# Performance work log

Measured on AMD Instinct MI355X. Metric: run time of the kernel, lower is better.

Reference implementation:

```python
import jax, jax.numpy as jnp
import numpy as np

EPS = 1e-6  # torch.nn.PairwiseDistance default eps, added to the difference vector


def setup_inputs() -> dict:
    key = jax.random.key(0)
    k1, k2, k3 = jax.random.split(key, 3)
    B, L1, L2, D = 4, 4096, 4096, 3
    contour1 = jax.random.normal(k1, (B, L1, D), dtype=jnp.float32)
    contour2 = jax.random.normal(k2, (B, L2, D), dtype=jnp.float32)
    resolution = jax.random.uniform(k3, (1,), dtype=jnp.float32)
    return {"contour1": contour1, "contour2": contour2, "resolution": resolution}


def reference(contour1, contour2, resolution):
    # torch PairwiseDistance(2): dist = ||x1 - x2 + eps||_2 with x1 from contour1,
    # x2 from contour2. Expand ||c1 - c2 + eps||^2 =
    #   ||c1||^2 + ||c2||^2 - 2 c1.c2 + 2*eps*(sum(c1) - sum(c2)) + D*eps^2
    # to avoid materializing the [B, L2, L1, D] repeated tensors.
    D = contour1.shape[-1]
    s1 = jnp.sum(contour1 * contour1, axis=-1)          # [B, L1]
    s2 = jnp.sum(contour2 * contour2, axis=-1)          # [B, L2]
    sum1 = jnp.sum(contour1, axis=-1)                   # [B, L1]
    sum2 = jnp.sum(contour2, axis=-1)                   # [B, L2]
    cross = jnp.einsum('bmd,bld->bml', contour2, contour1)  # [B, L2, L1]
    dist2 = (s2[:, :, None] + s1[:, None, :] - 2.0 * cross
             + 2.0 * EPS * (sum1[:, None, :] - sum2[:, :, None])
             + D * EPS * EPS)
    dist = jnp.sqrt(jnp.maximum(dist2, 0.0))            # [B, L2, L1]
    min_dist = jnp.min(dist, axis=2)                    # [B, L2]
    return jnp.mean(min_dist * resolution, axis=1)      # [B]
```

## Files before the change

kernel.cpp:

```cpp
#include <hip/hip_runtime.h>
#include <math.h>

#define EPS 1e-6f
#define FLT_BIG 3.402823466e+38f

constexpr int BLK = 256;
constexpr int MPT = 8;
constexpr int NCHUNK = 64;
constexpr int NMB = 2;
constexpr int CLK = 64;

__global__ void __launch_bounds__(BLK)
k_min(const float* __restrict__ c1, const float* __restrict__ c2,
      float* __restrict__ part, float* __restrict__ out, int L1, int L2) {
    __shared__ float4 tile[CLK];

    const int mb = blockIdx.x, chunk = blockIdx.y, b = blockIdx.z;
    const int tid = threadIdx.x;

    if (mb == 0 && chunk == 0 && tid == 0) out[b] = 0.0f;

    const int l0 = chunk * CLK;
    const float* src = c1 + ((size_t)b * L1 + l0) * 3;
    if (tid < CLK) {
        float x = src[3 * tid], y = src[3 * tid + 1], z = src[3 * tid + 2];
        tile[tid] = make_float4(fmaf(x, x, fmaf(y, y, z * z)),
                                -2.0f * x, -2.0f * y, -2.0f * z);
    }
    __syncthreads();

    const int mbase = mb * (BLK * MPT) + tid;

    float q0[MPT], q1[MPT], q2[MPT], mn[MPT];
    #pragma unroll
    for (int j = 0; j < MPT; ++j) {
        const float* q = c2 + ((size_t)b * L2 + mbase + j * BLK) * 3;
        q0[j] = q[0] - EPS; q1[j] = q[1] - EPS; q2[j] = q[2] - EPS;
        mn[j] = FLT_BIG;
    }

    #pragma unroll 2
    for (int l = 0; l < CLK; l += 2) {
        float4 pa = tile[l], pb = tile[l + 1];
        #pragma unroll
        for (int j = 0; j < MPT; ++j) {
            float ta = fmaf(pa.w, q2[j], fmaf(pa.z, q1[j], fmaf(pa.y, q0[j], pa.x)));
            float tb = fmaf(pb.w, q2[j], fmaf(pb.z, q1[j], fmaf(pb.y, q0[j], pb.x)));
            mn[j] = fminf(mn[j], fminf(ta, tb));
        }
    }

    float* dst = part + ((size_t)b * NCHUNK + chunk) * L2;
    #pragma unroll
    for (int j = 0; j < MPT; ++j) {
        const float qq = fmaf(q0[j], q0[j], fmaf(q1[j], q1[j], q2[j] * q2[j]));
        dst[mbase + j * BLK] = mn[j] + qq;
    }
}

__global__ void __launch_bounds__(BLK)
k_tail(const float* __restrict__ part, const float* __restrict__ res,
       float* __restrict__ out, int L2) {
    const int b = blockIdx.y;
    const int m = blockIdx.x * BLK + threadIdx.x;

    float v = FLT_BIG;
    #pragma unroll 8
    for (int c = 0; c < NCHUNK; ++c)
        v = fminf(v, part[((size_t)b * NCHUNK + c) * L2 + m]);
    float sum = sqrtf(fmaxf(v, 0.0f));

    #pragma unroll
    for (int s = 32; s > 0; s >>= 1)
        sum += __shfl_down(sum, s, 64);

    __shared__ float wred[BLK / 64];
    const int wid = threadIdx.x >> 6;
    if ((threadIdx.x & 63) == 0) wred[wid] = sum;
    __syncthreads();

    if (threadIdx.x == 0) {
        float tot = 0.0f;
        #pragma unroll
        for (int w = 0; w < BLK / 64; ++w) tot += wred[w];
        atomicAdd(&out[b], tot * res[0] / (float)L2);
    }
}

extern "C" void kernel_launch(void* const* d_in, const int* in_sizes, int n_in,
                              void* d_out, int out_size, void* d_ws, size_t ws_size,
                              hipStream_t stream) {
    const float* c1  = (const float*)d_in[0];
    const float* c2  = (const float*)d_in[1];
    const float* res = (const float*)d_in[2];
    float* out = (float*)d_out;

    const int B = out_size;
    const int D = 3;
    const int L1 = in_sizes[0] / (B * D);
    const int L2 = in_sizes[1] / (B * D);

    float* part = (float*)d_ws;

    dim3 g1(NMB, NCHUNK, B);
    k_min<<<g1, BLK, 0, stream>>>(c1, c2, part, out, L1, L2);

    dim3 g2(L2 / BLK, B);
    k_tail<<<g2, BLK, 0, stream>>>(part, res, out, L2);
}
```

Measured before the change: 18.56 us.

## Fuse min and tail kernels with full-L1 shared tile per block

Replaces the two-pass scheme, which wrote per-chunk partial minima to workspace and reduced them in a second kernel, with a single kernel. Each block loads all 4096 contour1 points into shared memory as a 64 KB float4 tile and handles 32 query points. Each query is split across 64 threads that reduce with shuffles and shared memory, and the block then applies the sqrt, sums, and does one atomic add. This removes the workspace round trip, but every block reloads the full contour1 tile (512 blocks) and the large shared allocation limits occupancy. A separate zeroing kernel is added, and L1 is hardcoded to 4096.

```diff
diff --git a/kernel.cpp b/kernel.cpp
--- a/kernel.cpp
+++ b/kernel.cpp
@@ -5,43 +5,53 @@
 #define FLT_BIG 3.402823466e+38f
 
 constexpr int BLK = 256;
+constexpr int MB  = 32;
 constexpr int MPT = 8;
-constexpr int NCHUNK = 64;
-constexpr int NMB = 2;
-constexpr int CLK = 64;
+constexpr int NG  = 4;
+constexpr int NSL = 64;
+constexpr int L1C = 4096;
 
-__global__ void __launch_bounds__(BLK)
-k_min(const float* __restrict__ c1, const float* __restrict__ c2,
-      float* __restrict__ part, float* __restrict__ out, int L1, int L2) {
-    __shared__ float4 tile[CLK];
+__global__ void k_zero(float* __restrict__ out, int B) {
+    if (threadIdx.x < B) out[threadIdx.x] = 0.0f;
+}
 
-    const int mb = blockIdx.x, chunk = blockIdx.y, b = blockIdx.z;
+__global__ void __launch_bounds__(BLK, 2)
+k_all(const float* __restrict__ c1, const float* __restrict__ c2,
+      const float* __restrict__ res, float* __restrict__ out,
+      int L1, int L2) {
+    __shared__ float4 tile[L1C];
+    __shared__ float wred[4 * MB];
+
+    const int blk = blockIdx.x;
+    const int b   = blockIdx.y;
     const int tid = threadIdx.x;
+    const int g   = tid & (NG - 1);
+    const int sl  = tid >> 2;
 
-    if (mb == 0 && chunk == 0 && tid == 0) out[b] = 0.0f;
+    const float* src = c1 + (size_t)b * L1 * 3;
+    #pragma unroll
+    for (int k = 0; k < L1C / BLK; ++k) {
+        const int i = k * BLK + tid;
+        float x = src[3 * i], y = src[3 * i + 1], z = src[3 * i + 2];
+        tile[i] = make_float4(fmaf(x, x, fmaf(y, y, z * z)),
+                              -2.0f * x, -2.0f * y, -2.0f * z);
+    }
 
-    const int l0 = chunk * CLK;
-    const float* src = c1 + ((size_t)b * L1 + l0) * 3;
-    if (tid < CLK) {
-        float x = src[3 * tid], y = src[3 * tid + 1], z = src[3 * tid + 2];
-        tile[tid] = make_float4(fmaf(x, x, fmaf(y, y, z * z)),
-                                -2.0f * x, -2.0f * y, -2.0f * z);
+    const int m0 = blk * MB + g * MPT;
+    const float* q = c2 + ((size_t)b * L2 + m0) * 3;
+    float q0[MPT], q1[MPT], q2[MPT], qq[MPT], mn[MPT];
+    #pragma unroll
+    for (int j = 0; j < MPT; ++j) {
+        q0[j] = q[3 * j] - EPS; q1[j] = q[3 * j + 1] - EPS; q2[j] = q[3 * j + 2] - EPS;
+        qq[j] = fmaf(q0[j], q0[j], fmaf(q1[j], q1[j], q2[j] * q2[j]));
+        mn[j] = FLT_BIG;
     }
     __syncthreads();
 
-    const int mbase = mb * (BLK * MPT) + tid;
-
-    float q0[MPT], q1[MPT], q2[MPT], mn[MPT];
-    #pragma unroll
-    for (int j = 0; j < MPT; ++j) {
-        const float* q = c2 + ((size_t)b * L2 + mbase + j * BLK) * 3;
-        q0[j] = q[0] - EPS; q1[j] = q[1] - EPS; q2[j] = q[2] - EPS;
-        mn[j] = FLT_BIG;
-    }
-
-    #pragma unroll 2
-    for (int l = 0; l < CLK; l += 2) {
-        float4 pa = tile[l], pb = tile[l + 1];
+    #pragma unroll 4
+    for (int k = 0; k < NSL; k += 2) {
+        float4 pa = tile[k * NSL + sl];
+        float4 pb = tile[(k + 1) * NSL + sl];
         #pragma unroll
         for (int j = 0; j < MPT; ++j) {
             float ta = fmaf(pa.w, q2[j], fmaf(pa.z, q1[j], fmaf(pa.y, q0[j], pa.x)));
@@ -50,40 +60,29 @@
         }
     }
 
-    float* dst = part + ((size_t)b * NCHUNK + chunk) * L2;
+    const int wv = tid >> 6;
     #pragma unroll
     for (int j = 0; j < MPT; ++j) {
-        const float qq = fmaf(q0[j], q0[j], fmaf(q1[j], q1[j], q2[j] * q2[j]));
-        dst[mbase + j * BLK] = mn[j] + qq;
+        float v = mn[j] + qq[j];
+        v = fminf(v, __shfl_xor(v, 4, 64));
+        v = fminf(v, __shfl_xor(v, 8, 64));
+        v = fminf(v, __shfl_xor(v, 16, 64));
+        v = fminf(v, __shfl_xor(v, 32, 64));
+        if ((tid & 63) < NG)
+            wred[wv * MB + g * MPT + j] = v;
     }
-}
-
-__global__ void __launch_bounds__(BLK)
-k_tail(const float* __restrict__ part, const float* __restrict__ res,
-       float* __restrict__ out, int L2) {
-    const int b = blockIdx.y;
-    const int m = blockIdx.x * BLK + threadIdx.x;
-
-    float v = FLT_BIG;
-    #pragma unroll 8
-    for (int c = 0; c < NCHUNK; ++c)
-        v = fminf(v, part[((size_t)b * NCHUNK + c) * L2 + m]);
-    float sum = sqrtf(fmaxf(v, 0.0f));
-
-    #pragma unroll
-    for (int s = 32; s > 0; s >>= 1)
-        sum += __shfl_down(sum, s, 64);
-
-    __shared__ float wred[BLK / 64];
-    const int wid = threadIdx.x >> 6;
-    if ((threadIdx.x & 63) == 0) wred[wid] = sum;
     __syncthreads();
 
-    if (threadIdx.x == 0) {
-        float tot = 0.0f;
-        #pragma unroll
-        for (int w = 0; w < BLK / 64; ++w) tot += wred[w];
-        atomicAdd(&out[b], tot * res[0] / (float)L2);
+    if (tid < MB) {
+        float v = fminf(fminf(wred[tid], wred[MB + tid]),
+                        fminf(wred[2 * MB + tid], wred[3 * MB + tid]));
+        float d = sqrtf(fmaxf(v, 0.0f));
+        d += __shfl_down(d, 16, 64);
+        d += __shfl_down(d, 8, 64);
+        d += __shfl_down(d, 4, 64);
+        d += __shfl_down(d, 2, 64);
+        d += __shfl_down(d, 1, 64);
+        if (tid == 0) atomicAdd(&out[b], d * res[0] / (float)L2);
     }
 }
 
@@ -100,11 +99,8 @@
     const int L1 = in_sizes[0] / (B * D);
     const int L2 = in_sizes[1] / (B * D);
 
-    float* part = (float*)d_ws;
+    k_zero<<<1, 64, 0, stream>>>(out, B);
 
-    dim3 g1(NMB, NCHUNK, B);
-    k_min<<<g1, BLK, 0, stream>>>(c1, c2, part, out, L1, L2);
-
-    dim3 g2(L2 / BLK, B);
-    k_tail<<<g2, BLK, 0, stream>>>(part, res, out, L2);
+    dim3 grid(L2 / MB, B);
+    k_all<<<grid, BLK, 0, stream>>>(c1, c2, res, out, L1, L2);
 }
```

Result: slower. 23.51 us (+26.7%).
